# Performance work log

Measured on AMD Instinct MI355X. Metric: run time of the kernel, lower is better.

Reference implementation:

```python
import jax, jax.numpy as jnp
import numpy as np

HEADS = 16
DIM_HEAD = 64
SCALE = DIM_HEAD ** -0.5
LN_EPS = 1e-5


def setup_inputs() -> dict:
    key = jax.random.key(0)
    k1, k2, k3 = jax.random.split(key, 3)
    b, s, d = 2, 2048, 1024
    inner = HEADS * DIM_HEAD
    x = jax.random.normal(k1, (b, s, d), dtype=jnp.float32)
    w_qkv = jax.random.normal(k2, (d, 3 * inner), dtype=jnp.float32) * (d ** -0.5)
    w_out = jax.random.normal(k3, (inner, d), dtype=jnp.float32) * (inner ** -0.5)
    return {
        "x": x,
        "ln_gamma": jnp.ones((d,), jnp.float32),
        "ln_beta": jnp.zeros((d,), jnp.float32),
        "w_qkv": w_qkv,
        "w_out": w_out,
        "b_out": jnp.zeros((d,), jnp.float32),
    }


def _layernorm(x, gamma, beta):
    mu = jnp.mean(x, axis=-1, keepdims=True)
    var = jnp.var(x, axis=-1, keepdims=True)
    return (x - mu) * jax.lax.rsqrt(var + LN_EPS) * gamma + beta


def reference(x, ln_gamma, ln_beta, w_qkv, w_out, b_out):
    b, s, d = x.shape
    xn = _layernorm(x, ln_gamma, ln_beta)
    qkv = xn @ w_qkv                       # [b, s, 3*inner]
    q, k, v = jnp.split(qkv, 3, axis=-1)
    def heads(t):
        return t.reshape(b, s, HEADS, DIM_HEAD).transpose(0, 2, 1, 3)  # [b, h, s, dh]
    q, k, v = heads(q), heads(k), heads(v)
    dots = jnp.einsum("bhqd,bhkd->bhqk", q, k) * SCALE   # [b, h, s, s]
    attn = jax.nn.softmax(dots, axis=-1)
    out = jnp.einsum("bhqk,bhkd->bhqd", attn, v)          # [b, h, s, dh]
    out = out.transpose(0, 2, 1, 3).reshape(b, s, HEADS * DIM_HEAD)
    return out @ w_out + b_out
```

## Files before the change

### kernel.cpp

```cpp
#include <hip/hip_runtime.h>
#include <hip/hip_bf16.h>
#include <stdint.h>

#define NH     16
#define DHEAD  64
#define SEQ    2048
#define DMODEL 1024
#define NBATCH 2
#define INNER  1024
#define QKVN   3072
#define ROWS   4096
#define ATT_QB 64
#define ATT_KB 64

typedef __attribute__((ext_vector_type(8))) __bf16 bf16x8;
typedef __attribute__((ext_vector_type(4))) float floatx4;

__device__ __forceinline__ unsigned short f2bf(float f) {
    union { __bf16 b; unsigned short u; } c; c.b = (__bf16)f; return c.u;
}

__device__ __forceinline__ float fexp2(float x) {
#if __has_builtin(__builtin_amdgcn_exp2f)
    return __builtin_amdgcn_exp2f(x);
#else
    float r; asm("v_exp_f32 %0, %1" : "=v"(r) : "v"(x)); return r;
#endif
}

typedef __attribute__((address_space(1))) void gvoid;
typedef __attribute__((address_space(3))) void lvoid;
__device__ __forceinline__ void gl_lds16(const void* g, void* l) {
    __builtin_amdgcn_global_load_lds((gvoid*)g, (lvoid*)l, 16, 0, 0);
}

__global__ __launch_bounds__(256) void transpose_f2b(
        const float* __restrict__ in, unsigned short* __restrict__ out,
        int rows, int cols) {
    __shared__ unsigned short tile[32][33];
    const int bx = blockIdx.x * 32, by = blockIdx.y * 32;
    const int tx = threadIdx.x & 31, ty = threadIdx.x >> 5;
    for (int i = ty; i < 32; i += 8)
        tile[i][tx] = f2bf(in[(size_t)(by + i) * cols + bx + tx]);
    __syncthreads();
    for (int i = ty; i < 32; i += 8)
        out[(size_t)(bx + i) * rows + by + tx] = tile[tx][i];
}

__global__ __launch_bounds__(256) void ln_kernel(
        const float* __restrict__ x,
        const float* __restrict__ gamma,
        const float* __restrict__ beta,
        unsigned short* __restrict__ xn) {
    __shared__ float red[4][2];
    const int row = blockIdx.x, t = threadIdx.x;
    const size_t base = (size_t)row * DMODEL + t * 4;
    float4 v = *(const float4*)(x + base);
    float s  = v.x + v.y + v.z + v.w;
    float ss = v.x*v.x + v.y*v.y + v.z*v.z + v.w*v.w;
    for (int off = 32; off >= 1; off >>= 1) {
        s  += __shfl_xor(s,  off);
        ss += __shfl_xor(ss, off);
    }
    const int w = t >> 6, lane = t & 63;
    if (lane == 0) { red[w][0] = s; red[w][1] = ss; }
    __syncthreads();
    if (t == 0) {
        float S  = red[0][0] + red[1][0] + red[2][0] + red[3][0];
        float SS = red[0][1] + red[1][1] + red[2][1] + red[3][1];
        float mu  = S * (1.f / DMODEL);
        float var = SS * (1.f / DMODEL) - mu * mu;
        red[0][0] = mu; red[0][1] = rsqrtf(var + 1e-5f);
    }
    __syncthreads();
    const float mu = red[0][0], rstd = red[0][1];
    float4 g = *(const float4*)(gamma + t * 4);
    float4 bb = *(const float4*)(beta + t * 4);
    ushort4 o;
    o.x = f2bf((v.x - mu) * rstd * g.x + bb.x);
    o.y = f2bf((v.y - mu) * rstd * g.y + bb.y);
    o.z = f2bf((v.z - mu) * rstd * g.z + bb.z);
    o.w = f2bf((v.w - mu) * rstd * g.w + bb.w);
    *(ushort4*)(xn + base) = o;
}

__global__ __launch_bounds__(256) void gemm_qkv(
        const unsigned short* __restrict__ A,
        const unsigned short* __restrict__ Bt,
        unsigned short* __restrict__ qP,
        unsigned short* __restrict__ kP,
        unsigned short* __restrict__ vT) {
    const int K = DMODEL;
    __shared__ __align__(16) unsigned short sA[128 * 32];
    __shared__ __align__(16) unsigned short sB[128 * 32];
    __shared__ __align__(16) unsigned short tb[2][64 * 72];
    const int t = threadIdx.x;
    const int mBase = blockIdx.y * 128, nBase = blockIdx.x * 128;
    const int w = t >> 6, lane = t & 63, quad = lane >> 4, l16 = lane & 15;
    const int wm = (w >> 1) * 64, wn = (w & 1) * 64;
    const int srow = t >> 2, sch = t & 3;
    floatx4 acc[4][4];
    for (int mi = 0; mi < 4; mi++)
        for (int ni = 0; ni < 4; ni++) acc[mi][ni] = (floatx4)0.f;

    for (int k0 = 0; k0 < K; k0 += 32) {
        #pragma unroll
        for (int c = 0; c < 2; c++) {
            const int row = c * 64 + srow;
            const int gcol = (sch ^ ((row >> 1) & 3)) * 8;
            gl_lds16(&A[(size_t)(mBase + row) * K + k0 + gcol], &sA[(c * 256 + w * 64) * 8]);
            gl_lds16(&Bt[(size_t)(nBase + row) * K + k0 + gcol], &sB[(c * 256 + w * 64) * 8]);
        }
        __syncthreads();
        bf16x8 af[4], bfv[4];
        #pragma unroll
        for (int mi = 0; mi < 4; mi++) {
            const int r = wm + mi * 16 + l16;
            af[mi] = *(const bf16x8*)&sA[r * 32 + (quad ^ ((r >> 1) & 3)) * 8];
        }
        #pragma unroll
        for (int ni = 0; ni < 4; ni++) {
            const int r = wn + ni * 16 + l16;
            bfv[ni] = *(const bf16x8*)&sB[r * 32 + (quad ^ ((r >> 1) & 3)) * 8];
        }
        #pragma unroll
        for (int mi = 0; mi < 4; mi++)
            #pragma unroll
            for (int ni = 0; ni < 4; ni++)
                acc[mi][ni] = __builtin_amdgcn_mfma_f32_16x16x32_bf16(
                    af[mi], bfv[ni], acc[mi][ni], 0, 0, 0);
        __syncthreads();
    }
    const int reg = nBase >> 10;
    if (reg == 2) {
        #pragma unroll
        for (int ni = 0; ni < 4; ni++) {
            const int col = nBase + wn + ni * 16 + l16;
            const int h = (col & 1023) >> 6, dh = col & 63;
            #pragma unroll
            for (int mi = 0; mi < 4; mi++) {
                const int row0 = mBase + wm + mi * 16 + quad * 4;
                const int b = row0 >> 11, s0 = row0 & 2047;
                ushort4 o;
                o.x = f2bf(acc[mi][ni][0]); o.y = f2bf(acc[mi][ni][1]);
                o.z = f2bf(acc[mi][ni][2]); o.w = f2bf(acc[mi][ni][3]);
                *(ushort4*)&vT[((size_t)(b * NH + h) * DHEAD + dh) * SEQ + s0] = o;
            }
        }
    } else {
        unsigned short* dst = (reg == 0) ? qP : kP;
        const float scl = (reg == 0) ? 0.18033688011112042f : 1.f;
        const int hh = ((nBase + wn) & 1023) >> 6;
        #pragma unroll
        for (int ph = 0; ph < 2; ph++) {
            if ((w >> 1) == ph) {
                unsigned short* tb_ = &tb[w & 1][0];
                #pragma unroll
                for (int mi = 0; mi < 4; mi++)
                    #pragma unroll
                    for (int ni = 0; ni < 4; ni++)
                        #pragma unroll
                        for (int i = 0; i < 4; i++)
                            tb_[(mi * 16 + quad * 4 + i) * 72 + ni * 16 + l16] =
                                f2bf(acc[mi][ni][i] * scl);
                asm volatile("s_waitcnt lgkmcnt(0)" ::: "memory");
                const int row_g = mBase + wm + lane;
                const int b = row_g >> 11, sr = row_g & 2047;
                unsigned short* orow = dst + ((size_t)(b * NH + hh) * SEQ + sr) * DHEAD;
                #pragma unroll
                for (int c = 0; c < 8; c++)
                    *(bf16x8*)&orow[c * 8] = *(const bf16x8*)&tb_[lane * 72 + c * 8];
            }
            __syncthreads();
        }
    }
}

__global__ __launch_bounds__(256) void gemm_out(
        const unsigned short* __restrict__ A,
        const unsigned short* __restrict__ Bt,
        float* __restrict__ C,
        const int M, const int N, const int K,
        const float* __restrict__ bias) {
    __shared__ __align__(16) unsigned short sA[128 * 32];
    __shared__ __align__(16) unsigned short sB[64 * 32];
    const int t = threadIdx.x;
    const int mBase = blockIdx.y * 128, nBase = blockIdx.x * 64;
    const int w = t >> 6, lane = t & 63, quad = lane >> 4, l16 = lane & 15;
    const int wm = (w >> 1) * 64, wn = (w & 1) * 32;
    const int srow = t >> 2, sch = t & 3;
    floatx4 acc[4][2];
    for (int mi = 0; mi < 4; mi++)
        for (int ni = 0; ni < 2; ni++) acc[mi][ni] = (floatx4)0.f;

    for (int k0 = 0; k0 < K; k0 += 32) {
        #pragma unroll
        for (int c = 0; c < 2; c++) {
            const int row = c * 64 + srow;
            const int gcol = (sch ^ ((row >> 1) & 3)) * 8;
            gl_lds16(&A[(size_t)(mBase + row) * K + k0 + gcol], &sA[(c * 256 + w * 64) * 8]);
        }
        {
            const int gcol = (sch ^ ((srow >> 1) & 3)) * 8;
            gl_lds16(&Bt[(size_t)(nBase + srow) * K + k0 + gcol], &sB[(w * 64) * 8]);
        }
        __syncthreads();
        bf16x8 af[4], bfv[2];
        #pragma unroll
        for (int mi = 0; mi < 4; mi++) {
            const int r = wm + mi * 16 + l16;
            af[mi] = *(const bf16x8*)&sA[r * 32 + (quad ^ ((r >> 1) & 3)) * 8];
        }
        #pragma unroll
        for (int ni = 0; ni < 2; ni++) {
            const int r = wn + ni * 16 + l16;
            bfv[ni] = *(const bf16x8*)&sB[r * 32 + (quad ^ ((r >> 1) & 3)) * 8];
        }
        #pragma unroll
        for (int mi = 0; mi < 4; mi++)
            #pragma unroll
            for (int ni = 0; ni < 2; ni++)
                acc[mi][ni] = __builtin_amdgcn_mfma_f32_16x16x32_bf16(
                    af[mi], bfv[ni], acc[mi][ni], 0, 0, 0);
        __syncthreads();
    }
    #pragma unroll
    for (int mi = 0; mi < 4; mi++)
        #pragma unroll
        for (int ni = 0; ni < 2; ni++) {
            const int col = nBase + wn + ni * 16 + l16;
            const float badd = bias ? bias[col] : 0.f;
            #pragma unroll
            for (int i = 0; i < 4; i++) {
                const int row = mBase + wm + mi * 16 + quad * 4 + i;
                C[(size_t)row * N + col] = acc[mi][ni][i] + badd;
            }
        }
}

__global__ __launch_bounds__(128, 2) void attn_kernel(
        const unsigned short* __restrict__ qP,
        const unsigned short* __restrict__ kP,
        const unsigned short* __restrict__ vT,
        unsigned short* __restrict__ aout) {
    __shared__ __align__(16) unsigned short sK[2][ATT_KB * 64];
    __shared__ __align__(16) unsigned short sV[2][ATT_KB * 64];
    __shared__ __align__(16) unsigned short sP[2][2][16 * 64];
    const int t = threadIdx.x, w = t >> 6, lane = t & 63;
    const int quad = lane >> 4, l16 = lane & 15;
    const int bid = blockIdx.x;
    const int xcd = bid & 7, slot = bid >> 3;
    const int bh = xcd * 4 + (slot >> 5);
    const int qb = slot & 31;
    const int b = bh >> 4, h = bh & 15;
    const int qbase = qb * ATT_QB + w * 32;
    const int swr = l16 & 7;

    bf16x8 aq[2][2];
    #pragma unroll
    for (int st = 0; st < 2; st++)
        #pragma unroll
        for (int hh = 0; hh < 2; hh++)
            aq[st][hh] = *(const bf16x8*)&qP[
                ((size_t)bh * SEQ + qbase + st * 16 + l16) * DHEAD + hh * 32 + quad * 8];

    floatx4 oac[2][4];
    float lS[2] = {0.f, 0.f};
    #pragma unroll
    for (int st = 0; st < 2; st++)
        #pragma unroll
        for (int c = 0; c < 4; c++) oac[st][c] = (floatx4)0.f;

    const unsigned short* kb = kP + (size_t)bh * SEQ * DHEAD;
    const unsigned short* vb = vT + (size_t)bh * DHEAD * SEQ;
    const int r8 = lane >> 3, sw8 = ((lane & 7) ^ r8) * 8;

    auto stage = [&](int it, int bi) {
        const int kv0 = it * ATT_KB;
        #pragma unroll
        for (int ii = 0; ii < 4; ii++) {
            const int row = w * 32 + ii * 8 + r8;
            gl_lds16(kb + (size_t)(kv0 + row) * DHEAD + sw8,
                     (void*)&sK[bi][(w * 32 + ii * 8) * 64]);
            gl_lds16(vb + (size_t)row * SEQ + kv0 + sw8,
                     (void*)&sV[bi][(w * 32 + ii * 8) * 64]);
        }
    };
    stage(0, 0);

    const int NIT = SEQ / ATT_KB;
    for (int it = 0; it < NIT; ++it) {
        __syncthreads();
        if (it + 1 < NIT) stage(it + 1, (it + 1) & 1);
        const unsigned short* sKb = &sK[it & 1][0];
        const unsigned short* sVb = &sV[it & 1][0];

        bf16x8 kf[4][2];
        #pragma unroll
        for (int c = 0; c < 4; c++)
            #pragma unroll
            for (int hh = 0; hh < 2; hh++)
                kf[c][hh] = *(const bf16x8*)&sKb[(c * 16 + l16) * 64 +
                                                 8 * (((hh << 2) | quad) ^ swr)];
        floatx4 sv[2][4];
        __builtin_amdgcn_s_setprio(1);
        #pragma unroll
        for (int st = 0; st < 2; st++)
            #pragma unroll
            for (int c = 0; c < 4; c++) {
                floatx4 a = (floatx4)0.f;
                a = __builtin_amdgcn_mfma_f32_16x16x32_bf16(kf[c][0], aq[st][0], a, 0, 0, 0);
                a = __builtin_amdgcn_mfma_f32_16x16x32_bf16(kf[c][1], aq[st][1], a, 0, 0, 0);
                sv[st][c] = a;
            }
        __builtin_amdgcn_s_setprio(0);
        #pragma unroll
        for (int st = 0; st < 2; st++) {
            float sum = 0.f;
            unsigned short* pb = (unsigned short*)&sP[w][st][0];
            #pragma unroll
            for (int c = 0; c < 4; c++) {
                float p0 = fexp2(sv[st][c][0]), p1 = fexp2(sv[st][c][1]);
                float p2 = fexp2(sv[st][c][2]), p3 = fexp2(sv[st][c][3]);
                sum += (p0 + p1) + (p2 + p3);
                ushort4 pk;
                pk.x = f2bf(p0); pk.y = f2bf(p1); pk.z = f2bf(p2); pk.w = f2bf(p3);
                *(ushort4*)&pb[l16 * 64 + 8 * ((((c << 1) | (quad >> 1))) ^ swr) + (quad & 1) * 4] = pk;
            }
            sum += __shfl_xor(sum, 16);
            sum += __shfl_xor(sum, 32);
            lS[st] += sum;
        }
        bf16x8 vf[4][2];
        #pragma unroll
        for (int c = 0; c < 4; c++)
            #pragma unroll
            for (int hh = 0; hh < 2; hh++)
                vf[c][hh] = *(const bf16x8*)&sVb[(c * 16 + l16) * 64 +
                                                 8 * (((hh << 2) | quad) ^ swr)];
        asm volatile("s_waitcnt lgkmcnt(0)" ::: "memory");
        #pragma unroll
        for (int st = 0; st < 2; st++) {
            const unsigned short* pb = (const unsigned short*)&sP[w][st][0];
            bf16x8 pf[2];
            #pragma unroll
            for (int hh = 0; hh < 2; hh++)
                pf[hh] = *(const bf16x8*)&pb[l16 * 64 + 8 * (((hh << 2) | quad) ^ swr)];
            __builtin_amdgcn_s_setprio(1);
            #pragma unroll
            for (int c = 0; c < 4; c++) {
                oac[st][c] = __builtin_amdgcn_mfma_f32_16x16x32_bf16(vf[c][0], pf[0], oac[st][c], 0, 0, 0);
                oac[st][c] = __builtin_amdgcn_mfma_f32_16x16x32_bf16(vf[c][1], pf[1], oac[st][c], 0, 0, 0);
            }
            __builtin_amdgcn_s_setprio(0);
        }
    }
    #pragma unroll
    for (int st = 0; st < 2; st++) {
        const float rl = 1.f / lS[st];
        unsigned short* orow = aout +
            ((size_t)(b * SEQ + qbase + st * 16 + l16)) * INNER + h * DHEAD;
        #pragma unroll
        for (int c = 0; c < 4; c++) {
            ushort4 o;
            o.x = f2bf(oac[st][c][0] * rl);
            o.y = f2bf(oac[st][c][1] * rl);
            o.z = f2bf(oac[st][c][2] * rl);
            o.w = f2bf(oac[st][c][3] * rl);
            *(ushort4*)&orow[c * 16 + quad * 4] = o;
        }
    }
}

extern "C" void kernel_launch(void* const* d_in, const int* in_sizes, int n_in,
                              void* d_out, int out_size, void* d_ws, size_t ws_size,
                              hipStream_t stream) {
    const float* x     = (const float*)d_in[0];
    const float* gamma = (const float*)d_in[1];
    const float* beta  = (const float*)d_in[2];
    const float* wqkv  = (const float*)d_in[3];
    const float* wout  = (const float*)d_in[4];
    const float* bout  = (const float*)d_in[5];
    float* out = (float*)d_out;

    unsigned short* ws     = (unsigned short*)d_ws;
    unsigned short* xn     = ws;
    unsigned short* wqkvT  = xn     + (size_t)ROWS * DMODEL;
    unsigned short* qPb    = wqkvT  + (size_t)QKVN * DMODEL;
    unsigned short* kPb    = qPb    + (size_t)NBATCH * NH * SEQ * DHEAD;
    unsigned short* vTb    = kPb    + (size_t)NBATCH * NH * SEQ * DHEAD;
    unsigned short* attnO  = vTb    + (size_t)NBATCH * NH * SEQ * DHEAD;
    unsigned short* woutT  = attnO  + (size_t)ROWS * INNER;

    transpose_f2b<<<dim3(QKVN / 32, DMODEL / 32), 256, 0, stream>>>(wqkv, wqkvT, DMODEL, QKVN);
    transpose_f2b<<<dim3(DMODEL / 32, INNER / 32), 256, 0, stream>>>(wout, woutT, INNER, DMODEL);
    ln_kernel<<<ROWS, 256, 0, stream>>>(x, gamma, beta, xn);
    gemm_qkv<<<dim3(QKVN / 128, ROWS / 128), 256, 0, stream>>>(xn, wqkvT, qPb, kPb, vTb);
    attn_kernel<<<dim3((SEQ / ATT_QB) * NBATCH * NH), 128, 0, stream>>>(
        qPb, kPb, vTb, attnO);
    gemm_out<<<dim3(DMODEL / 64, ROWS / 128), 256, 0, stream>>>(
        attnO, woutT, out, ROWS, DMODEL, INNER, bout);
}
```

Before: 217.4 us.

## Switch attention to 32x32x16 MFMA and keep P in registers via permlane swap

Rewrites the attention inner loop to use 32x32x16 bf16 MFMAs instead of 16x16x32, so each wave computes a 32-query by 64-key score tile with two accumulators. The softmax probabilities are packed to bf16 and rearranged across lane halves with v_permlane32_swap, letting them feed the PV MFMA directly from registers. This removes the shared-memory round trip for P and the lgkmcnt wait. It also reorders the K loads ahead of the next-tile prefetch. The cost is higher register pressure from the 32-float p array and the 16-wide accumulators, under a launch bound of 2 blocks.

```diff
diff --git a/kernel.cpp b/kernel.cpp
--- a/kernel.cpp
+++ b/kernel.cpp
@@ -15,9 +15,15 @@
 
 typedef __attribute__((ext_vector_type(8))) __bf16 bf16x8;
 typedef __attribute__((ext_vector_type(4))) float floatx4;
+typedef __attribute__((ext_vector_type(16))) float floatx16;
 
 __device__ __forceinline__ unsigned short f2bf(float f) {
     union { __bf16 b; unsigned short u; } c; c.b = (__bf16)f; return c.u;
+}
+
+__device__ __forceinline__ unsigned int pk2(float lo, float hi) {
+    union { ushort2 s; unsigned int u; } c;
+    c.s.x = f2bf(lo); c.s.y = f2bf(hi); return c.u;
 }
 
 __device__ __forceinline__ float fexp2(float x) {
@@ -245,31 +251,24 @@
         unsigned short* __restrict__ aout) {
     __shared__ __align__(16) unsigned short sK[2][ATT_KB * 64];
     __shared__ __align__(16) unsigned short sV[2][ATT_KB * 64];
-    __shared__ __align__(16) unsigned short sP[2][2][16 * 64];
     const int t = threadIdx.x, w = t >> 6, lane = t & 63;
-    const int quad = lane >> 4, l16 = lane & 15;
+    const int l32 = lane & 31, half = lane >> 5;
     const int bid = blockIdx.x;
     const int xcd = bid & 7, slot = bid >> 3;
     const int bh = xcd * 4 + (slot >> 5);
     const int qb = slot & 31;
     const int b = bh >> 4, h = bh & 15;
     const int qbase = qb * ATT_QB + w * 32;
-    const int swr = l16 & 7;
-
-    bf16x8 aq[2][2];
+
+    bf16x8 qf[4];
     #pragma unroll
-    for (int st = 0; st < 2; st++)
-        #pragma unroll
-        for (int hh = 0; hh < 2; hh++)
-            aq[st][hh] = *(const bf16x8*)&qP[
-                ((size_t)bh * SEQ + qbase + st * 16 + l16) * DHEAD + hh * 32 + quad * 8];
-
-    floatx4 oac[2][4];
-    float lS[2] = {0.f, 0.f};
-    #pragma unroll
-    for (int st = 0; st < 2; st++)
-        #pragma unroll
-        for (int c = 0; c < 4; c++) oac[st][c] = (floatx4)0.f;
+    for (int kd = 0; kd < 4; kd++)
+        qf[kd] = *(const bf16x8*)&qP[
+            ((size_t)bh * SEQ + qbase + l32) * DHEAD + kd * 16 + half * 8];
+
+    floatx16 oac[2];
+    oac[0] = (floatx16)0.f; oac[1] = (floatx16)0.f;
+    float lS = 0.f;
 
     const unsigned short* kb = kP + (size_t)bh * SEQ * DHEAD;
     const unsigned short* vb = vT + (size_t)bh * DHEAD * SEQ;
@@ -291,85 +290,87 @@
     const int NIT = SEQ / ATT_KB;
     for (int it = 0; it < NIT; ++it) {
         __syncthreads();
-        if (it + 1 < NIT) stage(it + 1, (it + 1) & 1);
-        const unsigned short* sKb = &sK[it & 1][0];
-        const unsigned short* sVb = &sV[it & 1][0];
-
-        bf16x8 kf[4][2];
-        #pragma unroll
-        for (int c = 0; c < 4; c++)
-            #pragma unroll
-            for (int hh = 0; hh < 2; hh++)
-                kf[c][hh] = *(const bf16x8*)&sKb[(c * 16 + l16) * 64 +
-                                                 8 * (((hh << 2) | quad) ^ swr)];
-        floatx4 sv[2][4];
+        const int bi = it & 1;
+        bf16x8 kf[2][4];
+        #pragma unroll
+        for (int tt = 0; tt < 2; tt++)
+            #pragma unroll
+            for (int kd = 0; kd < 4; kd++)
+                kf[tt][kd] = *(const bf16x8*)&sK[bi][(tt * 32 + l32) * 64 +
+                                                    8 * ((half + 2 * kd) ^ (l32 & 7))];
+        if (it + 1 < NIT) stage(it + 1, bi ^ 1);
+        bf16x8 vf[2][4];
+        #pragma unroll
+        for (int dt = 0; dt < 2; dt++)
+            #pragma unroll
+            for (int kd = 0; kd < 4; kd++)
+                vf[dt][kd] = *(const bf16x8*)&sV[bi][(dt * 32 + l32) * 64 +
+                                                    8 * ((half + 2 * kd) ^ (l32 & 7))];
+
+        floatx16 sv0 = (floatx16)0.f, sv1 = (floatx16)0.f;
         __builtin_amdgcn_s_setprio(1);
         #pragma unroll
-        for (int st = 0; st < 2; st++)
-            #pragma unroll
-            for (int c = 0; c < 4; c++) {
-                floatx4 a = (floatx4)0.f;
-                a = __builtin_amdgcn_mfma_f32_16x16x32_bf16(kf[c][0], aq[st][0], a, 0, 0, 0);
-                a = __builtin_amdgcn_mfma_f32_16x16x32_bf16(kf[c][1], aq[st][1], a, 0, 0, 0);
-                sv[st][c] = a;
+        for (int kd = 0; kd < 4; kd++)
+            sv0 = __builtin_amdgcn_mfma_f32_32x32x16_bf16(kf[0][kd], qf[kd], sv0, 0, 0, 0);
+        #pragma unroll
+        for (int kd = 0; kd < 4; kd++)
+            sv1 = __builtin_amdgcn_mfma_f32_32x32x16_bf16(kf[1][kd], qf[kd], sv1, 0, 0, 0);
+        __builtin_amdgcn_s_setprio(0);
+
+        float p[32];
+        #pragma unroll
+        for (int i = 0; i < 16; i++) p[i]      = fexp2(sv0[i]);
+        #pragma unroll
+        for (int i = 0; i < 16; i++) p[16 + i] = fexp2(sv1[i]);
+        {
+            float s0 = 0.f, s1 = 0.f;
+            #pragma unroll
+            for (int i = 0; i < 16; i++) { s0 += p[i]; s1 += p[16 + i]; }
+            float s = s0 + s1;
+            s += __shfl_xor(s, 32);
+            lS += s;
+        }
+
+        bf16x8 pf[4];
+        #pragma unroll
+        for (int tt = 0; tt < 2; tt++)
+            #pragma unroll
+            for (int e = 0; e < 2; e++) {
+                const int base = tt * 16 + e * 8;
+                unsigned int c01 = pk2(p[base + 0], p[base + 1]);
+                unsigned int c23 = pk2(p[base + 2], p[base + 3]);
+                unsigned int c45 = pk2(p[base + 4], p[base + 5]);
+                unsigned int c67 = pk2(p[base + 6], p[base + 7]);
+                asm("v_permlane32_swap_b32 %0, %1" : "+v"(c01), "+v"(c45));
+                asm("v_permlane32_swap_b32 %0, %1" : "+v"(c23), "+v"(c67));
+                union { unsigned int u[4]; bf16x8 v; } fr;
+                fr.u[0] = c01; fr.u[1] = c23; fr.u[2] = c45; fr.u[3] = c67;
+                pf[tt * 2 + e] = fr.v;
             }
+
+        __builtin_amdgcn_s_setprio(1);
+        #pragma unroll
+        for (int kd = 0; kd < 4; kd++)
+            oac[0] = __builtin_amdgcn_mfma_f32_32x32x16_bf16(vf[0][kd], pf[kd], oac[0], 0, 0, 0);
+        #pragma unroll
+        for (int kd = 0; kd < 4; kd++)
+            oac[1] = __builtin_amdgcn_mfma_f32_32x32x16_bf16(vf[1][kd], pf[kd], oac[1], 0, 0, 0);
         __builtin_amdgcn_s_setprio(0);
-        #pragma unroll
-        for (int st = 0; st < 2; st++) {
-            float sum = 0.f;
-            unsigned short* pb = (unsigned short*)&sP[w][st][0];
-            #pragma unroll
-            for (int c = 0; c < 4; c++) {
-                float p0 = fexp2(sv[st][c][0]), p1 = fexp2(sv[st][c][1]);
-                float p2 = fexp2(sv[st][c][2]), p3 = fexp2(sv[st][c][3]);
-                sum += (p0 + p1) + (p2 + p3);
-                ushort4 pk;
-                pk.x = f2bf(p0); pk.y = f2bf(p1); pk.z = f2bf(p2); pk.w = f2bf(p3);
-                *(ushort4*)&pb[l16 * 64 + 8 * ((((c << 1) | (quad >> 1))) ^ swr) + (quad & 1) * 4] = pk;
-            }
-            sum += __shfl_xor(sum, 16);
-            sum += __shfl_xor(sum, 32);
-            lS[st] += sum;
-        }
-        bf16x8 vf[4][2];
-        #pragma unroll
-        for (int c = 0; c < 4; c++)
-            #pragma unroll
-            for (int hh = 0; hh < 2; hh++)
-                vf[c][hh] = *(const bf16x8*)&sVb[(c * 16 + l16) * 64 +
-                                                 8 * (((hh << 2) | quad) ^ swr)];
-        asm volatile("s_waitcnt lgkmcnt(0)" ::: "memory");
-        #pragma unroll
-        for (int st = 0; st < 2; st++) {
-            const unsigned short* pb = (const unsigned short*)&sP[w][st][0];
-            bf16x8 pf[2];
-            #pragma unroll
-            for (int hh = 0; hh < 2; hh++)
-                pf[hh] = *(const bf16x8*)&pb[l16 * 64 + 8 * (((hh << 2) | quad) ^ swr)];
-            __builtin_amdgcn_s_setprio(1);
-            #pragma unroll
-            for (int c = 0; c < 4; c++) {
-                oac[st][c] = __builtin_amdgcn_mfma_f32_16x16x32_bf16(vf[c][0], pf[0], oac[st][c], 0, 0, 0);
-                oac[st][c] = __builtin_amdgcn_mfma_f32_16x16x32_bf16(vf[c][1], pf[1], oac[st][c], 0, 0, 0);
-            }
-            __builtin_amdgcn_s_setprio(0);
-        }
-    }
+    }
+
+    const float rl = 1.f / lS;
+    unsigned short* orow = aout + ((size_t)(b * SEQ + qbase + l32)) * INNER + h * DHEAD;
     #pragma unroll
-    for (int st = 0; st < 2; st++) {
-        const float rl = 1.f / lS[st];
-        unsigned short* orow = aout +
-            ((size_t)(b * SEQ + qbase + st * 16 + l16)) * INNER + h * DHEAD;
-        #pragma unroll
-        for (int c = 0; c < 4; c++) {
+    for (int dt = 0; dt < 2; dt++)
+        #pragma unroll
+        for (int g = 0; g < 4; g++) {
             ushort4 o;
-            o.x = f2bf(oac[st][c][0] * rl);
-            o.y = f2bf(oac[st][c][1] * rl);
-            o.z = f2bf(oac[st][c][2] * rl);
-            o.w = f2bf(oac[st][c][3] * rl);
-            *(ushort4*)&orow[c * 16 + quad * 4] = o;
-        }
-    }
+            o.x = f2bf(oac[dt][g * 4 + 0] * rl);
+            o.y = f2bf(oac[dt][g * 4 + 1] * rl);
+            o.z = f2bf(oac[dt][g * 4 + 2] * rl);
+            o.w = f2bf(oac[dt][g * 4 + 3] * rl);
+            *(ushort4*)&orow[dt * 32 + g * 8 + half * 4] = o;
+        }
 }
 
 extern "C" void kernel_launch(void* const* d_in, const int* in_sizes, int n_in,
```

New measurement: 214.7 us. Within noise of the previous version (-1.3%).
